# Kernel optimization log

Measured on AMD Instinct MI355X. Metric: run time of the kernel, lower is better.

## Reference

```python
import jax, jax.numpy as jnp
from jax import lax
import numpy as np

B, N, T, F = 2, 100, 15, 6
K, H = 4, 128          # edge_types, n_hid
E = N * (N - 1)        # fully connected off-diagonal graph


def setup_inputs() -> dict:
    key = jax.random.key(0)
    ks = jax.random.split(key, 24)
    s = 0.1
    data = jax.random.normal(ks[0], (B, N, T, F), jnp.float32)
    rel_type = jax.random.uniform(ks[1], (B, E, K), jnp.float32)
    off = ~np.eye(N, dtype=bool)
    recv_idx, send_idx = np.where(off)
    eye = np.eye(N, dtype=np.float32)
    rel_rec = jnp.asarray(eye[recv_idx])    # [E, N]
    rel_send = jnp.asarray(eye[send_idx])   # [E, N]
    inp = {
        'data': data, 'rel_type': rel_type,
        'rel_rec': rel_rec, 'rel_send': rel_send,
        'pred_steps': 1,
        # message MLPs, stacked over edge types (weights stored [in, out])
        'W1': jax.random.normal(ks[2], (K, 2 * H, H), jnp.float32) * s,
        'b1': jax.random.normal(ks[3], (K, H), jnp.float32) * s,
        'W2': jax.random.normal(ks[4], (K, H, H), jnp.float32) * s,
        'b2': jax.random.normal(ks[5], (K, H), jnp.float32) * s,
        # GRU-style gates (hidden_* have no bias in the torch module)
        'Whr': jax.random.normal(ks[6], (H, H), jnp.float32) * s,
        'Whi': jax.random.normal(ks[7], (H, H), jnp.float32) * s,
        'Whh': jax.random.normal(ks[8], (H, H), jnp.float32) * s,
        'Wir': jax.random.normal(ks[9], (F, H), jnp.float32) * s,
        'bir': jax.random.normal(ks[10], (H,), jnp.float32) * s,
        'Wii': jax.random.normal(ks[11], (F, H), jnp.float32) * s,
        'bii': jax.random.normal(ks[12], (H,), jnp.float32) * s,
        'Win': jax.random.normal(ks[13], (F, H), jnp.float32) * s,
        'bin_': jax.random.normal(ks[14], (H,), jnp.float32) * s,
        # output MLP
        'Wo1': jax.random.normal(ks[15], (H, H), jnp.float32) * s,
        'bo1': jax.random.normal(ks[16], (H,), jnp.float32) * s,
        'Wo2': jax.random.normal(ks[17], (H, H), jnp.float32) * s,
        'bo2': jax.random.normal(ks[18], (H,), jnp.float32) * s,
        'Wo3': jax.random.normal(ks[19], (H, F), jnp.float32) * s,
        'bo3': jax.random.normal(ks[20], (F,), jnp.float32) * s,
    }
    return inp


def _forward(data, rel_type, rel_rec, rel_send, pred_steps,
             W1, b1, W2, b2, Whr, Whi, Whh,
             Wir, bir, Wii, bii, Win, bin_,
             Wo1, bo1, Wo2, bo2, Wo3, bo3):
    inputs = jnp.swapaxes(data, 1, 2)            # [B, T, N, F]
    Bn, Tn, Nn, Fn = inputs.shape
    norm = jnp.asarray(W1.shape[0], inputs.dtype)  # edge_types (skip_first=False)
    hidden0 = jnp.zeros((Bn, Nn, Whr.shape[0]), inputs.dtype)

    def step_fn(carry, xs):
        hidden, prev_pred = carry
        gt, step = xs
        ins = jnp.where(step % pred_steps == 0, gt, prev_pred)  # [B, N, F]
        recv = jnp.einsum('en,bnh->beh', rel_rec, hidden)
        send = jnp.einsum('en,bnh->beh', rel_send, hidden)
        pre_msg = jnp.concatenate([send, recv], axis=-1)        # [B, E, 2H]
        # all edge-type message MLPs fused into batched einsums
        m1 = jnp.tanh(jnp.einsum('bei,kih->bekh', pre_msg, W1) + b1)
        m2 = jnp.tanh(jnp.einsum('bekh,khj->bekj', m1, W2) + b2)
        all_msgs = jnp.einsum('bekh,bek->beh', m2, rel_type) / norm
        # aggregate messages onto receiving nodes; torch divides by inputs.size(2)=F
        agg = jnp.einsum('beh,en->bnh', all_msgs, rel_rec) / Fn  # [B, N, H]
        r = jax.nn.sigmoid(ins @ Wir + bir + agg @ Whr)
        i = jax.nn.sigmoid(ins @ Wii + bii + agg @ Whi)
        n = jnp.tanh(ins @ Win + bin_ + r * (agg @ Whh))
        hidden_new = (1.0 - i) * n + i * hidden
        p = jax.nn.relu(hidden_new @ Wo1 + bo1)
        p = jax.nn.relu(p @ Wo2 + bo2)
        pred = ins + (p @ Wo3 + bo3)
        return (hidden_new, pred), pred

    xs = (jnp.swapaxes(inputs[:, :-1], 0, 1), jnp.arange(Tn - 1))
    (_, _), preds = lax.scan(step_fn, (hidden0, inputs[:, 0]), xs)
    preds = jnp.swapaxes(preds, 0, 1)   # [B, T-1, N, F]
    return jnp.swapaxes(preds, 1, 2)    # [B, N, T-1, F]


def reference(data, rel_type, rel_rec, rel_send, pred_steps,
              W1, b1, W2, b2, Whr, Whi, Whh,
              Wir, bir, Wii, bii, Win, bin_,
              Wo1, bo1, Wo2, bo2, Wo3, bo3):
    return _forward(data, rel_type, rel_rec, rel_send, pred_steps,
                    W1, b1, W2, b2, Whr, Whi, Whh,
                    Wir, bir, Wii, bii, Win, bin_,
                    Wo1, bo1, Wo2, bo2, Wo3, bo3)
```

## Files before the change

### kernel.cpp

```cpp
#include <hip/hip_runtime.h>
#include <math.h>

#define BB 2
#define NN 100
#define TT 15
#define FF 6
#define KK 4
#define HH 128
#define EE 9900
#define EPN 99
#define NSTEP 14
#define TILE_E 64

__device__ __forceinline__ float fast_tanh(float x) {
    float e = __expf(2.0f * x);
    return 1.0f - __fdividef(2.0f, 1.0f + e);
}
__device__ __forceinline__ float fast_sig(float x) {
    return __fdividef(1.0f, 1.0f + __expf(-x));
}

__global__ __launch_bounds__(256) void k_init(
    const float* __restrict__ b1,
    float* __restrict__ hidden,
    float* __restrict__ agg4,
    float* __restrict__ Hs,
    float* __restrict__ Hr)
{
    int i = blockIdx.x * 256 + threadIdx.x;
    if (i < BB * NN * HH) hidden[i] = 0.f;
    agg4[i] = 0.f;
    int k  = (i >> 7) & 3;
    int hh = i & 127;
    Hs[i] = 0.f;
    Hr[i] = b1[k * HH + hh];
}

__global__ __launch_bounds__(256) void k_edge(
    const float* __restrict__ Hs,
    const float* __restrict__ Hr,
    const float* __restrict__ W2,
    const float* __restrict__ b2,
    const float* __restrict__ rel_type,
    float* __restrict__ agg4)
{
    const int tile = blockIdx.x;
    const int b    = blockIdx.y;
    const int k    = blockIdx.z;
    const int e0   = tile * TILE_E;
    const int t    = threadIdx.x;
    const int hg   = t & 15;
    const int eg   = t >> 4;
    const int cA   = hg * 4;
    const int cB   = 64 + hg * 4;

    __shared__ __align__(16) float m1[TILE_E][132];
    __shared__ __align__(16) float w2c[32][132];
    __shared__ int s_send[TILE_E], s_recv[TILE_E];

    if (t < TILE_E) {
        int e = e0 + t;
        if (e >= EE) e = EE - 1;
        int r = e / EPN;
        int j = e - r * EPN;
        s_recv[t] = r;
        s_send[t] = j + (j >= r ? 1 : 0);
    }
    __syncthreads();

    const float4* Hs4 = (const float4*)Hs;
    const float4* Hr4 = (const float4*)Hr;
#pragma unroll
    for (int rep = 0; rep < 8; ++rep) {
        int idx = rep * 256 + t;
        int el  = idx >> 5;
        int f4  = idx & 31;
        int s   = s_send[el];
        int r   = s_recv[el];
        float4 a = Hs4[((b * NN + s) * KK + k) * 32 + f4];
        float4 c = Hr4[((b * NN + r) * KK + k) * 32 + f4];
        float4 v;
        v.x = fast_tanh(a.x + c.x);
        v.y = fast_tanh(a.y + c.y);
        v.z = fast_tanh(a.z + c.z);
        v.w = fast_tanh(a.w + c.w);
        *(float4*)&m1[el][f4 * 4] = v;
    }

    int   el[4], erecv[4];
    float relw[4];
    const float scale = 1.0f / (KK * FF);
#pragma unroll
    for (int ei = 0; ei < 4; ++ei) {
        int l = eg + 16 * ei;
        el[ei] = l;
        int e = e0 + l;
        bool valid = (e < EE);
        if (!valid) e = EE - 1;
        erecv[ei] = s_recv[l];
        relw[ei]  = valid ? rel_type[(b * EE + e) * KK + k] * scale : 0.f;
    }

    const float4* W2f4 = (const float4*)(W2 + k * HH * HH);

    float acc[4][8] = {};
    for (int jc = 0; jc < 4; ++jc) {
        __syncthreads();
#pragma unroll
        for (int rep = 0; rep < 4; ++rep) {
            int s   = rep * 256 + t;
            int row = s >> 5;
            int c4  = s & 31;
            *(float4*)&w2c[row][c4 * 4] = W2f4[(jc * 32 + row) * 32 + c4];
        }
        __syncthreads();
#pragma unroll
        for (int js = 0; js < 8; ++js) {
            float4 wA[4], wB[4];
#pragma unroll
            for (int jj = 0; jj < 4; ++jj) {
                wA[jj] = *(const float4*)&w2c[js * 4 + jj][cA];
                wB[jj] = *(const float4*)&w2c[js * 4 + jj][cB];
            }
#pragma unroll
            for (int ei = 0; ei < 4; ++ei) {
                float4 mv = *(const float4*)&m1[el[ei]][jc * 32 + js * 4];
                float* A = acc[ei];
                A[0] = fmaf(mv.x, wA[0].x, fmaf(mv.y, wA[1].x, fmaf(mv.z, wA[2].x, fmaf(mv.w, wA[3].x, A[0]))));
                A[1] = fmaf(mv.x, wA[0].y, fmaf(mv.y, wA[1].y, fmaf(mv.z, wA[2].y, fmaf(mv.w, wA[3].y, A[1]))));
                A[2] = fmaf(mv.x, wA[0].z, fmaf(mv.y, wA[1].z, fmaf(mv.z, wA[2].z, fmaf(mv.w, wA[3].z, A[2]))));
                A[3] = fmaf(mv.x, wA[0].w, fmaf(mv.y, wA[1].w, fmaf(mv.z, wA[2].w, fmaf(mv.w, wA[3].w, A[3]))));
                A[4] = fmaf(mv.x, wB[0].x, fmaf(mv.y, wB[1].x, fmaf(mv.z, wB[2].x, fmaf(mv.w, wB[3].x, A[4]))));
                A[5] = fmaf(mv.x, wB[0].y, fmaf(mv.y, wB[1].y, fmaf(mv.z, wB[2].y, fmaf(mv.w, wB[3].y, A[5]))));
                A[6] = fmaf(mv.x, wB[0].z, fmaf(mv.y, wB[1].z, fmaf(mv.z, wB[2].z, fmaf(mv.w, wB[3].z, A[6]))));
                A[7] = fmaf(mv.x, wB[0].w, fmaf(mv.y, wB[1].w, fmaf(mv.z, wB[2].w, fmaf(mv.w, wB[3].w, A[7]))));
            }
        }
    }

    float b2k[8];
    *(float4*)&b2k[0] = *(const float4*)&b2[k * HH + cA];
    *(float4*)&b2k[4] = *(const float4*)&b2[k * HH + cB];

    const int rA = s_recv[0];
    const int rB = s_recv[TILE_E - 1];
    float sumA[8] = {}, sumB[8] = {};
#pragma unroll
    for (int ei = 0; ei < 4; ++ei) {
        bool isA = (erecv[ei] == rA);
#pragma unroll
        for (int h = 0; h < 8; ++h) {
            float v = relw[ei] * fast_tanh(acc[ei][h] + b2k[h]);
            if (isA) sumA[h] += v; else sumB[h] += v;
        }
    }

    float* red  = &m1[0][0];
    float* aggk = agg4 + ((size_t)(k * BB + b)) * NN * HH;
    __syncthreads();
    *(float4*)&red[eg * 128 + cA] = make_float4(sumA[0], sumA[1], sumA[2], sumA[3]);
    *(float4*)&red[eg * 128 + cB] = make_float4(sumA[4], sumA[5], sumA[6], sumA[7]);
    __syncthreads();
    if (t < HH) {
        float s = 0.f;
#pragma unroll
        for (int y = 0; y < 16; ++y) s += red[y * 128 + t];
        atomicAdd(&aggk[rA * HH + t], s);
    }
    if (rB != rA) {
        __syncthreads();
        *(float4*)&red[eg * 128 + cA] = make_float4(sumB[0], sumB[1], sumB[2], sumB[3]);
        *(float4*)&red[eg * 128 + cB] = make_float4(sumB[4], sumB[5], sumB[6], sumB[7]);
        __syncthreads();
        if (t < HH) {
            float s = 0.f;
#pragma unroll
            for (int y = 0; y < 16; ++y) s += red[y * 128 + t];
            atomicAdd(&aggk[rB * HH + t], s);
        }
    }
}

__global__ __launch_bounds__(512) void k_gru_out(
    const float* __restrict__ data,
    float* __restrict__ agg4,
    float* __restrict__ hidden,
    const float* __restrict__ W1,  const float* __restrict__ b1,
    const float* __restrict__ Whr, const float* __restrict__ Whi,
    const float* __restrict__ Whh,
    const float* __restrict__ Wir, const float* __restrict__ bir,
    const float* __restrict__ Wii, const float* __restrict__ bii,
    const float* __restrict__ Win, const float* __restrict__ bin_,
    const float* __restrict__ Wo1, const float* __restrict__ bo1,
    const float* __restrict__ Wo2, const float* __restrict__ bo2,
    const float* __restrict__ Wo3, const float* __restrict__ bo3,
    float* __restrict__ Hs,
    float* __restrict__ Hr,
    float* __restrict__ out,
    const int* __restrict__ ps_ptr, int step)
{
    const int bn = blockIdx.x;
    const int t  = threadIdx.x;
    const int tt = t & 127;
    const int q  = t >> 7;

    __shared__ float sa[HH], sh[HH], p1b[HH], p2b[HH], insb[8];
    __shared__ float ap[4][HH];
    __shared__ float gp[3][4][HH];
    __shared__ float mp[4][HH];
    __shared__ float pp[16][HH];

    {
        size_t idx = ((size_t)q * BB * NN + bn) * HH + tt;
        ap[q][tt] = agg4[idx];
        agg4[idx] = 0.f;
    }
    if (t < FF) {
        int ps = ps_ptr[0];
        bool use_gt = (ps <= 1) || (step % ps == 0);
        int prev = (step > 0) ? (step - 1) : 0;
        float gt = data[(bn * TT + step) * FF + t];
        float pv = out[(bn * NSTEP + prev) * FF + t];
        insb[t] = use_gt ? gt : pv;
    }
    __syncthreads();
    if (t < HH) sa[t] = ap[0][t] + ap[1][t] + ap[2][t] + ap[3][t];
    __syncthreads();

    {
        const int j0 = q * 32;
        float pr = 0.f, pi = 0.f, ph = 0.f;
#pragma unroll 8
        for (int jj = 0; jj < 32; ++jj) {
            int j = j0 + jj;
            float a = sa[j];
            pr = fmaf(a, Whr[j * HH + tt], pr);
            pi = fmaf(a, Whi[j * HH + tt], pi);
            ph = fmaf(a, Whh[j * HH + tt], ph);
        }
        gp[0][q][tt] = pr; gp[1][q][tt] = pi; gp[2][q][tt] = ph;
    }
    __syncthreads();

    if (t < HH) {
        float ar = gp[0][0][t] + gp[0][1][t] + gp[0][2][t] + gp[0][3][t];
        float ai = gp[1][0][t] + gp[1][1][t] + gp[1][2][t] + gp[1][3][t];
        float ah = gp[2][0][t] + gp[2][1][t] + gp[2][2][t] + gp[2][3][t];
        float xr = bir[t], xi = bii[t], xn = bin_[t];
#pragma unroll
        for (int f = 0; f < FF; ++f) {
            float v = insb[f];
            xr = fmaf(v, Wir[f * HH + t], xr);
            xi = fmaf(v, Wii[f * HH + t], xi);
            xn = fmaf(v, Win[f * HH + t], xn);
        }
        float r  = fast_sig(xr + ar);
        float i  = fast_sig(xi + ai);
        float n  = fast_tanh(xn + r * ah);
        float hnew = (1.f - i) * n + i * hidden[bn * HH + t];
        hidden[bn * HH + t] = hnew;
        sh[t] = hnew;
    }
    __syncthreads();

    {
        const int j0 = q * 32;
        float a1 = 0.f;
#pragma unroll 8
        for (int jj = 0; jj < 32; ++jj) { int j = j0 + jj; a1 = fmaf(sh[j], Wo1[j * HH + tt], a1); }
        mp[q][tt] = a1;
    }
    __syncthreads();
    if (t < HH) p1b[t] = fmaxf(mp[0][t] + mp[1][t] + mp[2][t] + mp[3][t] + bo1[t], 0.f);
    __syncthreads();
    {
        const int j0 = q * 32;
        float a2 = 0.f;
#pragma unroll 8
        for (int jj = 0; jj < 32; ++jj) { int j = j0 + jj; a2 = fmaf(p1b[j], Wo2[j * HH + tt], a2); }
        mp[q][tt] = a2;
    }
    __syncthreads();
    if (t < HH) p2b[t] = fmaxf(mp[0][t] + mp[1][t] + mp[2][t] + mp[3][t] + bo2[t], 0.f);
    __syncthreads();

    if (t < FF) {
        float o = bo3[t];
#pragma unroll 4
        for (int j = 0; j < HH; ++j) o = fmaf(p2b[j], Wo3[j * FF + t], o);
        out[(bn * NSTEP + step) * FF + t] = insb[t] + o;
    }

    {
#pragma unroll
        for (int i = 0; i < 4; ++i) {
            int c     = 4 * q + i;
            int plane = c >> 1;
            int half  = c & 1;
            const float* Wp = W1 + (size_t)plane * HH * HH + tt;
            const int j0 = half * 64;
            float acc = 0.f;
#pragma unroll 8
            for (int jj = 0; jj < 64; ++jj) {
                int j = j0 + jj;
                acc = fmaf(sh[j], Wp[j * HH], acc);
            }
            pp[c][tt] = acc;
        }
    }
    __syncthreads();
    for (int o = t; o < 1024; o += 512) {
        int plane = o >> 7;
        int col   = o & 127;
        float v = pp[plane * 2][col] + pp[plane * 2 + 1][col];
        int kk = plane >> 1, which = plane & 1;
        if (which == 0) Hs[(bn * KK + kk) * HH + col] = v;
        else            Hr[(bn * KK + kk) * HH + col] = v + b1[kk * HH + col];
    }
}

extern "C" void kernel_launch(void* const* d_in, const int* in_sizes, int n_in,
                              void* d_out, int out_size, void* d_ws, size_t ws_size,
                              hipStream_t stream) {
    const float* data     = (const float*)d_in[0];
    const float* rel_type = (const float*)d_in[1];
    const int*   ps_ptr   = (const int*)d_in[4];
    const float* W1   = (const float*)d_in[5];
    const float* b1   = (const float*)d_in[6];
    const float* W2   = (const float*)d_in[7];
    const float* b2   = (const float*)d_in[8];
    const float* Whr  = (const float*)d_in[9];
    const float* Whi  = (const float*)d_in[10];
    const float* Whh  = (const float*)d_in[11];
    const float* Wir  = (const float*)d_in[12];
    const float* bir  = (const float*)d_in[13];
    const float* Wii  = (const float*)d_in[14];
    const float* bii  = (const float*)d_in[15];
    const float* Win  = (const float*)d_in[16];
    const float* bin_ = (const float*)d_in[17];
    const float* Wo1  = (const float*)d_in[18];
    const float* bo1  = (const float*)d_in[19];
    const float* Wo2  = (const float*)d_in[20];
    const float* bo2  = (const float*)d_in[21];
    const float* Wo3  = (const float*)d_in[22];
    const float* bo3  = (const float*)d_in[23];

    float* out = (float*)d_out;

    float* ws     = (float*)d_ws;
    float* hidden = ws;
    float* Hs     = ws + 25600;
    float* Hr     = ws + 128000;
    float* agg4   = ws + 230400;

    k_init<<<400, 256, 0, stream>>>(b1, hidden, agg4, Hs, Hr);

    const int ntile = (EE + TILE_E - 1) / TILE_E;
    dim3 egrid(ntile, BB, KK);

    for (int step = 0; step < NSTEP; ++step) {
        k_edge<<<egrid, 256, 0, stream>>>(Hs, Hr, W2, b2, rel_type, agg4);
        k_gru_out<<<BB * NN, 512, 0, stream>>>(data, agg4, hidden,
                                               W1, b1,
                                               Whr, Whi, Whh,
                                               Wir, bir, Wii, bii, Win, bin_,
                                               Wo1, bo1, Wo2, bo2, Wo3, bo3,
                                               Hs, Hr, out, ps_ptr, step);
    }
}
```

Baseline: 968.9 us.

## Double-buffer W2 chunks in LDS via async global_load_lds in edge kernel

Replaces the register-staged, synchronous loads of W2 tiles in the edge-message kernel with direct global-to-LDS async loads into two 16-row buffers. The next chunk is prefetched while the current one is consumed, so weight-fetch latency overlaps with the FMA loop. This also drops the padded LDS layout (132 to 128 columns) for the m1 and W2 tiles, which may add LDS bank conflicts on the m1 row reads. Correctness depends on __syncthreads waiting for the outstanding LDS-direct loads.

After: 1.035 ms. 1.07x slower.

```diff
diff --git a/kernel.cpp b/kernel.cpp
--- a/kernel.cpp
+++ b/kernel.cpp
@@ -11,6 +11,8 @@
 #define EPN 99
 #define NSTEP 14
 #define TILE_E 64
+#define CHUNK 16
+#define NCHUNK 8
 
 __device__ __forceinline__ float fast_tanh(float x) {
     float e = __expf(2.0f * x);
@@ -18,6 +20,12 @@
 }
 __device__ __forceinline__ float fast_sig(float x) {
     return __fdividef(1.0f, 1.0f + __expf(-x));
+}
+
+__device__ __forceinline__ void load_lds16(const float4* g, float4* l) {
+    __builtin_amdgcn_global_load_lds(
+        (const __attribute__((address_space(1))) void*)g,
+        (__attribute__((address_space(3))) void*)l, 16, 0, 0);
 }
 
 __global__ __launch_bounds__(256) void k_init(
@@ -54,8 +62,8 @@
     const int cA   = hg * 4;
     const int cB   = 64 + hg * 4;
 
-    __shared__ __align__(16) float m1[TILE_E][132];
-    __shared__ __align__(16) float w2c[32][132];
+    __shared__ __align__(16) float m1s[TILE_E * HH];
+    __shared__ __align__(16) float w2c[2][CHUNK * HH];
     __shared__ int s_send[TILE_E], s_recv[TILE_E];
 
     if (t < TILE_E) {
@@ -67,6 +75,11 @@
         s_send[t] = j + (j >= r ? 1 : 0);
     }
     __syncthreads();
+
+    const float4* W2f4 = (const float4*)(W2 + k * HH * HH);
+
+    load_lds16(W2f4 + t,       (float4*)w2c[0] + t);
+    load_lds16(W2f4 + 256 + t, (float4*)w2c[0] + 256 + t);
 
     const float4* Hs4 = (const float4*)Hs;
     const float4* Hr4 = (const float4*)Hr;
@@ -84,7 +97,7 @@
         v.y = fast_tanh(a.y + c.y);
         v.z = fast_tanh(a.z + c.z);
         v.w = fast_tanh(a.w + c.w);
-        *(float4*)&m1[el][f4 * 4] = v;
+        *(float4*)&m1s[el * HH + f4 * 4] = v;
     }
 
     int   el[4], erecv[4];
@@ -101,30 +114,28 @@
         relw[ei]  = valid ? rel_type[(b * EE + e) * KK + k] * scale : 0.f;
     }
 
-    const float4* W2f4 = (const float4*)(W2 + k * HH * HH);
-
+    __syncthreads();
+
+    const float4* m1f4 = (const float4*)m1s;
     float acc[4][8] = {};
-    for (int jc = 0; jc < 4; ++jc) {
-        __syncthreads();
-#pragma unroll
-        for (int rep = 0; rep < 4; ++rep) {
-            int s   = rep * 256 + t;
-            int row = s >> 5;
-            int c4  = s & 31;
-            *(float4*)&w2c[row][c4 * 4] = W2f4[(jc * 32 + row) * 32 + c4];
-        }
-        __syncthreads();
-#pragma unroll
-        for (int js = 0; js < 8; ++js) {
+    for (int c = 0; c < NCHUNK; ++c) {
+        if (c + 1 < NCHUNK) {
+            float4* nb = (float4*)w2c[(c + 1) & 1];
+            load_lds16(W2f4 + (c + 1) * 512 + t,       nb + t);
+            load_lds16(W2f4 + (c + 1) * 512 + 256 + t, nb + 256 + t);
+        }
+        const float4* wf = (const float4*)w2c[c & 1];
+#pragma unroll
+        for (int js = 0; js < 4; ++js) {
             float4 wA[4], wB[4];
 #pragma unroll
             for (int jj = 0; jj < 4; ++jj) {
-                wA[jj] = *(const float4*)&w2c[js * 4 + jj][cA];
-                wB[jj] = *(const float4*)&w2c[js * 4 + jj][cB];
+                wA[jj] = wf[(js * 4 + jj) * 32 + hg];
+                wB[jj] = wf[(js * 4 + jj) * 32 + 16 + hg];
             }
 #pragma unroll
             for (int ei = 0; ei < 4; ++ei) {
-                float4 mv = *(const float4*)&m1[el[ei]][jc * 32 + js * 4];
+                float4 mv = m1f4[el[ei] * 32 + c * 4 + js];
                 float* A = acc[ei];
                 A[0] = fmaf(mv.x, wA[0].x, fmaf(mv.y, wA[1].x, fmaf(mv.z, wA[2].x, fmaf(mv.w, wA[3].x, A[0]))));
                 A[1] = fmaf(mv.x, wA[0].y, fmaf(mv.y, wA[1].y, fmaf(mv.z, wA[2].y, fmaf(mv.w, wA[3].y, A[1]))));
@@ -136,6 +147,7 @@
                 A[7] = fmaf(mv.x, wB[0].w, fmaf(mv.y, wB[1].w, fmaf(mv.z, wB[2].w, fmaf(mv.w, wB[3].w, A[7]))));
             }
         }
+        __syncthreads();
     }
 
     float b2k[8];
@@ -155,9 +167,8 @@
         }
     }
 
-    float* red  = &m1[0][0];
+    float* red  = m1s;
     float* aggk = agg4 + ((size_t)(k * BB + b)) * NN * HH;
-    __syncthreads();
     *(float4*)&red[eg * 128 + cA] = make_float4(sumA[0], sumA[1], sumA[2], sumA[3]);
     *(float4*)&red[eg * 128 + cB] = make_float4(sumA[4], sumA[5], sumA[6], sumA[7]);
     __syncthreads();
```
